# Optimization experiments

Measured on AMD Instinct MI355X. Metric: run time of the kernel, lower is better.

The kernel has to match this reference:

```python
import jax, jax.numpy as jnp
import numpy as np
from jax import lax

GAMMA = 0.1  # fixed RBF bandwidth from LearnableRBFInfluence


def setup_inputs() -> dict:
    key = jax.random.key(0)
    k1, k2, k3, k4 = jax.random.split(key, 4)
    B, H, W = 2, 256, 256
    NUM_FILTERS, KS, NUM_BASIS = 48, 7, 31
    u_log = jax.random.normal(k1, (B, 1, H, W), jnp.float32)
    f_log = jax.random.normal(k2, (B, 1, H, W), jnp.float32)
    filters = jax.random.normal(k3, (NUM_FILTERS, 1, KS, KS), jnp.float32) * 0.05
    rbf_weights = jax.random.normal(k4, (NUM_FILTERS, NUM_BASIS), jnp.float32) * 0.05
    lambda_param = jnp.float32(0.1)
    return {"u_log": u_log, "f_log": f_log, "filters": filters,
            "rbf_weights": rbf_weights, "lambda_param": lambda_param}


def reference(u_log, f_log, filters, rbf_weights, lambda_param):
    # Batched form of the per-filter loop:
    #   conv[i] = conv2d(u, k_i)  ->  one grouped conv with 48 output channels
    num_basis = rbf_weights.shape[1]
    mu = jnp.linspace(-1.0, 1.0, num_basis).astype(u_log.dtype)  # [K]

    dn = lax.conv_dimension_numbers(u_log.shape, filters.shape, ('NCHW', 'OIHW', 'NCHW'))
    conv = lax.conv_general_dilated(u_log, filters, (1, 1), 'SAME',
                                    dimension_numbers=dn)  # [B,48,H,W]

    # RBF influence, per filter channel c: phi = sum_k w[c,k] * exp(-(conv-mu_k)^2/(2 g^2))
    diff = conv[..., None] - mu                              # [B,48,H,W,K]
    rbf = jnp.exp(-(diff * diff) / (2.0 * GAMMA * GAMMA))
    phi = jnp.einsum('bchwk,ck->bchw', rbf, rbf_weights)     # [B,48,H,W]

    # Per-filter conv2d(phi_i, flip(k_i)) summed over i == single conv
    # with OIHW weight [1,48,7,7] built from spatially-flipped filters.
    kT = jnp.flip(filters, axis=(2, 3)).transpose(1, 0, 2, 3)  # [1,48,7,7]
    dn2 = lax.conv_dimension_numbers(phi.shape, kT.shape, ('NCHW', 'OIHW', 'NCHW'))
    diffusion = lax.conv_general_dilated(phi, kT, (1, 1), 'SAME',
                                         dimension_numbers=dn2)  # [B,1,H,W]

    reaction = lambda_param * (u_log - f_log)
    return u_log - diffusion - reaction
```

## Files before the change

kernel.cpp:

```cpp
#include <hip/hip_runtime.h>

#define HH 256
#define WW 256
#define NPIX (2 * HH * WW)
#define NC 48
#define NB 31
#define TP 192

#define OTY 32
#define OTX 64
#define PTY 38
#define PTX 70
#define PSTR2 76
#define UTY 44
#define UTX 76
#define USTR2 84
#define N1ITEM 684

#define OT 32
#define PT 38
#define PSTR 44
#define UT 44
#define USTR 52


__global__ __launch_bounds__(256)
void tnrd_table(const float* __restrict__ wr, float2* __restrict__ tab)
{
    const int ch = blockIdx.x;
    const float* rc = wr + ch * NB;
    for (int j = threadIdx.x; j < TP; j += 256) {
        float v0 = 0.f, v1 = 0.f;
        float x0 = fmaf((float)j, 1.0f / 64.0f, -1.5f);
        float x1 = x0 + 1.0f / 64.0f;
        #pragma unroll
        for (int k = 0; k < NB; ++k) {
            float mu = -1.f + (float)k * (1.f / 15.f);
            float d0 = x0 - mu, d1 = x1 - mu;
            float w = rc[k];
            v0 = fmaf(w, __expf(-50.f * d0 * d0), v0);
            v1 = fmaf(w, __expf(-50.f * d1 * d1), v1);
        }
        tab[ch * TP + j] = make_float2(v0, v1 - v0);
    }
}

#define F1STEP(WI, s0, s1, s2, s3)                                      \
    { float fa = wa[WI], fb = wb[WI];                                   \
      a0 = fmaf(s0, fa, a0); a1 = fmaf(s1, fa, a1);                     \
      a2 = fmaf(s2, fa, a2); a3 = fmaf(s3, fa, a3);                     \
      b0 = fmaf(s0, fb, b0); b1 = fmaf(s1, fb, b1);                     \
      b2 = fmaf(s2, fb, b2); b3 = fmaf(s3, fb, b3); }

#define F1ROW(WA, WB, q0, q1, q2)                                       \
    { const float* wa = (WA); const float* wb = (WB);                   \
      F1STEP(0, q0.x, q0.y, q0.z, q0.w)                                 \
      F1STEP(1, q0.y, q0.z, q0.w, q1.x)                                 \
      F1STEP(2, q0.z, q0.w, q1.x, q1.y)                                 \
      F1STEP(3, q0.w, q1.x, q1.y, q1.z)                                 \
      F1STEP(4, q1.x, q1.y, q1.z, q1.w)                                 \
      F1STEP(5, q1.y, q1.z, q1.w, q2.x)                                 \
      F1STEP(6, q1.z, q1.w, q2.x, q2.y) }

#define LERP1(res, aval, T)                                             \
    { float t_ = fminf(fmaxf(fmaf(aval, 64.f, 96.f), 0.f), 191.999f);   \
      float fj_ = floorf(t_);                                           \
      float2 e_ = (T)[(int)fj_];               \
      res = fmaf(t_ - fj_, e_.y, e_.x); }

#define C2STEPG(WI, s0, s1, s2, s3, t0, t1, t2, t3)                     \
    { float fa = wra[WI], fb = wrb[WI];                                 \
      q0 = fmaf(s0, fa, q0); q1 = fmaf(s1, fa, q1);                     \
      q2 = fmaf(s2, fa, q2); q3 = fmaf(s3, fa, q3);                     \
      q0 = fmaf(t0, fb, q0); q1 = fmaf(t1, fb, q1);                     \
      q2 = fmaf(t2, fb, q2); q3 = fmaf(t3, fb, q3); }

#define C2SWEEP()                                                       \
    C2STEPG(6, A0.x, A0.y, A0.z, A0.w, B0.x, B0.y, B0.z, B0.w)          \
    C2STEPG(5, A0.y, A0.z, A0.w, A1.x, B0.y, B0.z, B0.w, B1.x)          \
    C2STEPG(4, A0.z, A0.w, A1.x, A1.y, B0.z, B0.w, B1.x, B1.y)          \
    C2STEPG(3, A0.w, A1.x, A1.y, A1.z, B0.w, B1.x, B1.y, B1.z)          \
    C2STEPG(2, A1.x, A1.y, A1.z, A1.w, B1.x, B1.y, B1.z, B1.w)          \
    C2STEPG(1, A1.y, A1.z, A1.w, A2.x, B1.y, B1.z, B1.w, B2.x)          \
    C2STEPG(0, A1.z, A1.w, A2.x, A2.y, B1.z, B1.w, B2.x, B2.y)

__global__ __launch_bounds__(256, 4)
void tnrd_main_2x(const float* __restrict__ u,
                  const float* __restrict__ wf,
                  const float2* __restrict__ tab,
                  float* __restrict__ part)
{
    __shared__ __align__(16) float u_s[UTY * USTR2];
    __shared__ __align__(16) float phi_s[2][PTY * PSTR2];

    const int tid = threadIdx.x;
    const int bx = blockIdx.x, by = blockIdx.y;
    const int b = blockIdx.z / 24, g = blockIdx.z % 24;
    const int c0 = g * 2;

    const int uy0 = by * OTY - 6, ux0 = bx * OTX - 6;
    const float* ub = u + b * (HH * WW);
    for (int i = tid; i < UTY * USTR2; i += 256) {
        int r = i / USTR2, c = i - r * USTR2;
        int gy = uy0 + r, gx = ux0 + c;
        float v = 0.f;
        if (c < UTX && (unsigned)gy < HH && (unsigned)gx < WW)
            v = ub[gy * WW + gx];
        u_s[i] = v;
    }
    __syncthreads();

    const int py0 = by * OTY - 3, px0 = bx * OTX - 3;

    {
        const float* wA = wf + c0 * 49;
        const float* wB = wA + 49;
        const float2* tA = tab + c0 * TP;
        const float2* tB = tA + TP;
        for (int p = 0; p < 3; ++p) {
            const int gi = tid + p * 256;
            if (gi < N1ITEM) {
                const int pr = gi / 18, pc = (gi % 18) * 4;
                float a0 = 0.f, a1 = 0.f, a2 = 0.f, a3 = 0.f;
                float b0 = 0.f, b1 = 0.f, b2 = 0.f, b3 = 0.f;
                const float* bptr = &u_s[pr * USTR2 + pc];

                float4 c0v = *(const float4*)(bptr);
                float4 c1v = *(const float4*)(bptr + 4);
                float2 c2v = *(const float2*)(bptr + 8);
                #pragma unroll 1
                for (int dy = 0; dy < 6; ++dy) {
                    const float* nr = bptr + (dy + 1) * USTR2;
                    float4 n0 = *(const float4*)(nr);
                    float4 n1 = *(const float4*)(nr + 4);
                    float2 n2 = *(const float2*)(nr + 8);
                    F1ROW(wA + dy * 7, wB + dy * 7, c0v, c1v, c2v)
                    c0v = n0; c1v = n1; c2v = n2;
                }
                F1ROW(wA + 42, wB + 42, c0v, c1v, c2v)

                const int gy = py0 + pr;
                const bool rowok = (unsigned)gy < HH;
                const bool ok0 = rowok && (unsigned)(px0 + pc + 0) < WW;
                const bool ok1 = rowok && (unsigned)(px0 + pc + 1) < WW;
                const bool ok2 = rowok && (unsigned)(px0 + pc + 2) < WW;
                const bool ok3 = rowok && (unsigned)(px0 + pc + 3) < WW;
                float pA0, pA1, pA2, pA3, pB0, pB1, pB2, pB3;
                LERP1(pA0, a0, tA) LERP1(pB0, b0, tB)
                LERP1(pA1, a1, tA) LERP1(pB1, b1, tB)
                LERP1(pA2, a2, tA) LERP1(pB2, b2, tB)
                LERP1(pA3, a3, tA) LERP1(pB3, b3, tB)
                pA0 = ok0 ? pA0 : 0.f;  pB0 = ok0 ? pB0 : 0.f;
                pA1 = ok1 ? pA1 : 0.f;  pB1 = ok1 ? pB1 : 0.f;
                pA2 = ok2 ? pA2 : 0.f;  pB2 = ok2 ? pB2 : 0.f;
                pA3 = ok3 ? pA3 : 0.f;  pB3 = ok3 ? pB3 : 0.f;
                *(float4*)(&phi_s[0][pr * PSTR2 + pc]) =
                    make_float4(pA0, pA1, pA2, pA3);
                *(float4*)(&phi_s[1][pr * PSTR2 + pc]) =
                    make_float4(pB0, pB1, pB2, pB3);
            }
        }
    }
    __syncthreads();

    {
        const int tr = tid >> 4;
        const int ox = (tid & 15) * 4;
        const float* wA = wf + c0 * 49;
        const float* wB = wA + 49;
        float o00 = 0.f, o01 = 0.f, o02 = 0.f, o03 = 0.f;
        float o10 = 0.f, o11 = 0.f, o12 = 0.f, o13 = 0.f;

        #pragma unroll
        for (int dyt = 0; dyt < 8; ++dyt) {
            const float* rA = &phi_s[0][(2 * tr + dyt) * PSTR2 + ox];
            const float* rB = &phi_s[1][(2 * tr + dyt) * PSTR2 + ox];
            const float4 A0 = *(const float4*)(rA);
            const float4 A1 = *(const float4*)(rA + 4);
            const float2 A2 = *(const float2*)(rA + 8);
            const float4 B0 = *(const float4*)(rB);
            const float4 B1 = *(const float4*)(rB + 4);
            const float2 B2 = *(const float2*)(rB + 8);
            if (dyt < 7) {
                const float* wra = wA + (6 - dyt) * 7;
                const float* wrb = wB + (6 - dyt) * 7;
                float &q0 = o00, &q1 = o01, &q2 = o02, &q3 = o03;
                C2SWEEP()
            }
            if (dyt > 0) {
                const float* wra = wA + (7 - dyt) * 7;
                const float* wrb = wB + (7 - dyt) * 7;
                float &q0 = o10, &q1 = o11, &q2 = o12, &q3 = o13;
                C2SWEEP()
            }
        }

        const int gy0 = by * OTY + 2 * tr, gx = bx * OTX + ox;
        float* dst = part + (size_t)g * NPIX + b * (HH * WW) + gy0 * WW + gx;
        *reinterpret_cast<float4*>(dst)      = make_float4(o00, o01, o02, o03);
        *reinterpret_cast<float4*>(dst + WW) = make_float4(o10, o11, o12, o13);
    }
}

#define C2STEP(WI, s0, s1, s2, s3, t0, t1, t2, t3)                      \
    { float fa = wra[WI], fb = wrb[WI];                                 \
      o0 = fmaf(s0, fa, o0); o1 = fmaf(s1, fa, o1);                     \
      o2 = fmaf(s2, fa, o2); o3 = fmaf(s3, fa, o3);                     \
      o0 = fmaf(t0, fb, o0); o1 = fmaf(t1, fb, o1);                     \
      o2 = fmaf(t2, fb, o2); o3 = fmaf(t3, fb, o3); }

template<int CPG>
__global__ __launch_bounds__(256, 6)
void tnrd_main(const float* __restrict__ u,
               const float* __restrict__ wf,
               const float2* __restrict__ tab,
               float* __restrict__ part)
{
    constexpr int NGRP = NC / CPG;
    constexpr int NPASS = CPG / 2;
    __shared__ __align__(16) float u_s[UT * USTR];
    __shared__ __align__(16) float phi_s[2][PT * PSTR];

    const int tid = threadIdx.x;
    const int bx = blockIdx.x, by = blockIdx.y;
    const int b = blockIdx.z / NGRP, g = blockIdx.z % NGRP;
    const int c0g = g * CPG;

    const int uy0 = by * OT - 6, ux0 = bx * OT - 6;
    const float* ub = u + b * (HH * WW);
    for (int i = tid; i < UT * USTR; i += 256) {
        int r = i / USTR, c = i - r * USTR;
        int gy = uy0 + r, gx = ux0 + c;
        float v = 0.f;
        if (c < UT && (unsigned)gy < HH && (unsigned)gx < WW)
            v = ub[gy * WW + gx];
        u_s[i] = v;
    }
    __syncthreads();

    const int oy = tid >> 3;
    const int ox0 = (tid & 7) * 4;
    float o0 = 0.f, o1 = 0.f, o2 = 0.f, o3 = 0.f;
    const int py0 = by * OT - 3, px0 = bx * OT - 3;

    auto conv1_pass = [&](int cp, float* __restrict__ bufA,
                          float* __restrict__ bufB) {
        const float* wA = wf + (c0g + 2 * cp) * 49;
        const float* wB = wA + 49;
        const float2* tA = tab + (c0g + 2 * cp) * TP;
        const float2* tB = tA + TP;
        for (int p = 0; p < 2; ++p) {
            const int gi = tid + p * 256;
            if (gi < PT * 10) {
                const int pr = gi % PT, pc = (gi / PT) * 4;
                float a0 = 0.f, a1 = 0.f, a2 = 0.f, a3 = 0.f;
                float b0 = 0.f, b1 = 0.f, b2 = 0.f, b3 = 0.f;
                const float* bptr = &u_s[pr * USTR + pc];
                float4 c0 = *(const float4*)(bptr);
                float4 c1 = *(const float4*)(bptr + 4);
                float2 c2 = *(const float2*)(bptr + 8);
                #pragma unroll 1
                for (int dy = 0; dy < 6; ++dy) {
                    const float* nr = bptr + (dy + 1) * USTR;
                    float4 n0 = *(const float4*)(nr);
                    float4 n1 = *(const float4*)(nr + 4);
                    float2 n2 = *(const float2*)(nr + 8);
                    F1ROW(wA + dy * 7, wB + dy * 7, c0, c1, c2)
                    c0 = n0; c1 = n1; c2 = n2;
                }
                F1ROW(wA + 42, wB + 42, c0, c1, c2)
                const int gy = py0 + pr;
                const bool rowok = (unsigned)gy < HH;
                const bool ok0 = rowok && (unsigned)(px0 + pc + 0) < WW;
                const bool ok1 = rowok && (unsigned)(px0 + pc + 1) < WW;
                const bool ok2 = rowok && (unsigned)(px0 + pc + 2) < WW;
                const bool ok3 = rowok && (unsigned)(px0 + pc + 3) < WW;
                float pA0, pA1, pA2, pA3, pB0, pB1, pB2, pB3;
                LERP1(pA0, a0, tA) LERP1(pB0, b0, tB)
                LERP1(pA1, a1, tA) LERP1(pB1, b1, tB)
                LERP1(pA2, a2, tA) LERP1(pB2, b2, tB)
                LERP1(pA3, a3, tA) LERP1(pB3, b3, tB)
                pA0 = ok0 ? pA0 : 0.f;  pB0 = ok0 ? pB0 : 0.f;
                pA1 = ok1 ? pA1 : 0.f;  pB1 = ok1 ? pB1 : 0.f;
                pA2 = ok2 ? pA2 : 0.f;  pB2 = ok2 ? pB2 : 0.f;
                pA3 = ok3 ? pA3 : 0.f;  pB3 = ok3 ? pB3 : 0.f;
                *(float4*)(bufA + pr * PSTR + pc) =
                    make_float4(pA0, pA1, pA2, pA3);
                *(float4*)(bufB + pr * PSTR + pc) =
                    make_float4(pB0, pB1, pB2, pB3);
            }
        }
    };

    #pragma unroll 1
    for (int pass = 0; pass < NPASS; ++pass) {
        conv1_pass(pass, phi_s[0], phi_s[1]);
        __syncthreads();
        const float* wA = wf + (c0g + 2 * pass) * 49;
        const float* wB = wA + 49;
        const float* pA = phi_s[0];
        const float* pB = phi_s[1];
        for (int dy = 0; dy < 7; ++dy) {
            const float* rA = pA + (oy + dy) * PSTR + ox0;
            const float* rB = pB + (oy + dy) * PSTR + ox0;
            const float4 A0 = *(const float4*)(rA);
            const float4 A1 = *(const float4*)(rA + 4);
            const float2 A2 = *(const float2*)(rA + 8);
            const float4 B0 = *(const float4*)(rB);
            const float4 B1 = *(const float4*)(rB + 4);
            const float2 B2 = *(const float2*)(rB + 8);
            const float* wra = wA + (6 - dy) * 7;
            const float* wrb = wB + (6 - dy) * 7;
            C2STEP(6, A0.x, A0.y, A0.z, A0.w, B0.x, B0.y, B0.z, B0.w)
            C2STEP(5, A0.y, A0.z, A0.w, A1.x, B0.y, B0.z, B0.w, B1.x)
            C2STEP(4, A0.z, A0.w, A1.x, A1.y, B0.z, B0.w, B1.x, B1.y)
            C2STEP(3, A0.w, A1.x, A1.y, A1.z, B0.w, B1.x, B1.y, B1.z)
            C2STEP(2, A1.x, A1.y, A1.z, A1.w, B1.x, B1.y, B1.z, B1.w)
            C2STEP(1, A1.y, A1.z, A1.w, A2.x, B1.y, B1.z, B1.w, B2.x)
            C2STEP(0, A1.z, A1.w, A2.x, A2.y, B1.z, B1.w, B2.x, B2.y)
        }
        if (pass < NPASS - 1) __syncthreads();
    }

    const int gy = by * OT + oy, gx = bx * OT + ox0;
    float4 v4 = make_float4(o0, o1, o2, o3);
    *reinterpret_cast<float4*>(part + (size_t)g * NPIX + b * (HH * WW)
                               + gy * WW + gx) = v4;
}

template<int NGRP>
__global__ __launch_bounds__(256)
void combine_kernel(const float* __restrict__ u,
                    const float* __restrict__ f,
                    const float* __restrict__ lam,
                    const float* __restrict__ part,
                    float* __restrict__ out)
{
    int i = blockIdx.x * 256 + threadIdx.x;
    float d = 0.f;
    #pragma unroll
    for (int g = 0; g < NGRP; ++g) d += part[g * NPIX + i];
    float lv = lam[0];
    float uv = u[i];
    float fv = f[i];
    out[i] = uv - d - lv * (uv - fv);
}

extern "C" void kernel_launch(void* const* d_in, const int* in_sizes, int n_in,
                              void* d_out, int out_size, void* d_ws, size_t ws_size,
                              hipStream_t stream) {
    const float* u    = (const float*)d_in[0];
    const float* f    = (const float*)d_in[1];
    const float* filt = (const float*)d_in[2];
    const float* rbfw = (const float*)d_in[3];
    const float* lam  = (const float*)d_in[4];
    float* out = (float*)d_out;
    float* part = (float*)d_ws;
    float2* tabg = (float2*)d_out;

    tnrd_table<<<NC, 256, 0, stream>>>(rbfw, tabg);
    if (ws_size >= (size_t)24 * NPIX * sizeof(float)) {
        tnrd_main_2x<<<dim3(WW / OTX, HH / OTY, 48), 256, 0, stream>>>(
            u, filt, tabg, part);
        combine_kernel<24><<<512, 256, 0, stream>>>(u, f, lam, part, out);
    } else if (ws_size >= (size_t)12 * NPIX * sizeof(float)) {
        tnrd_main<4><<<dim3(8, 8, 24), 256, 0, stream>>>(u, filt, tabg, part);
        combine_kernel<12><<<512, 256, 0, stream>>>(u, f, lam, part, out);
    } else {
        tnrd_main<8><<<dim3(8, 8, 12), 256, 0, stream>>>(u, filt, tabg, part);
        combine_kernel<6><<<512, 256, 0, stream>>>(u, f, lam, part, out);
    }
}
```

Before: 101.9 us.

## Pre-pad input in global memory and read conv1 directly from it

A fused kernel now builds the RBF lookup table and writes a zero-padded copy of u into workspace. The main kernel drops its shared-memory staging of u and the barrier after it, and reads the first convolution's inputs from the padded global buffer with no bounds checks. Freeing that shared memory lets occupancy rise from 4 to 6 blocks per SM. The cost is an extra global write and read of the padded image, plus first-conv loads that now rely on L1/L2 caching instead of LDS.

```diff
diff --git a/kernel.cpp b/kernel.cpp
--- a/kernel.cpp
+++ b/kernel.cpp
@@ -10,12 +10,11 @@
 #define OTY 32
 #define OTX 64
 #define PTY 38
-#define PTX 70
 #define PSTR2 76
-#define UTY 44
-#define UTX 76
-#define USTR2 84
 #define N1ITEM 684
+
+#define PADW 272
+#define PADN (2 * PADW * PADW)
 
 #define OT 32
 #define PT 38
@@ -23,6 +22,42 @@
 #define UT 44
 #define USTR 52
 
+
+__global__ __launch_bounds__(256)
+void tnrd_table_pad(const float* __restrict__ wr,
+                    const float* __restrict__ u,
+                    float2* __restrict__ tab,
+                    float* __restrict__ upad)
+{
+    const int bid = blockIdx.x;
+    {
+        const int i = bid * 256 + threadIdx.x;
+        const int img = i / (PADW * PADW);
+        const int rem = i - img * (PADW * PADW);
+        const int py = rem / PADW, px = rem - py * PADW;
+        const int gy = py - 6, gx = px - 6;
+        float v = 0.f;
+        if ((unsigned)gy < HH && (unsigned)gx < WW)
+            v = u[img * (HH * WW) + gy * WW + gx];
+        upad[i] = v;
+    }
+    if (bid < NC && threadIdx.x < TP) {
+        const int j = threadIdx.x;
+        const float* rc = wr + bid * NB;
+        float v0 = 0.f, v1 = 0.f;
+        float x0 = fmaf((float)j, 1.0f / 64.0f, -1.5f);
+        float x1 = x0 + 1.0f / 64.0f;
+        #pragma unroll
+        for (int k = 0; k < NB; ++k) {
+            float mu = -1.f + (float)k * (1.f / 15.f);
+            float d0 = x0 - mu, d1 = x1 - mu;
+            float w = rc[k];
+            v0 = fmaf(w, __expf(-50.f * d0 * d0), v0);
+            v1 = fmaf(w, __expf(-50.f * d1 * d1), v1);
+        }
+        tab[bid * TP + j] = make_float2(v0, v1 - v0);
+    }
+}
 
 __global__ __launch_bounds__(256)
 void tnrd_table(const float* __restrict__ wr, float2* __restrict__ tab)
@@ -52,7 +87,7 @@
       b0 = fmaf(s0, fb, b0); b1 = fmaf(s1, fb, b1);                     \
       b2 = fmaf(s2, fb, b2); b3 = fmaf(s3, fb, b3); }
 
-#define F1ROW(WA, WB, q0, q1, q2)                                       \
+#define F1ROW(WA, WB, q0, q1, q2)                                      \
     { const float* wa = (WA); const float* wb = (WB);                   \
       F1STEP(0, q0.x, q0.y, q0.z, q0.w)                                 \
       F1STEP(1, q0.y, q0.z, q0.w, q1.x)                                 \
@@ -84,31 +119,18 @@
     C2STEPG(1, A1.y, A1.z, A1.w, A2.x, B1.y, B1.z, B1.w, B2.x)          \
     C2STEPG(0, A1.z, A1.w, A2.x, A2.y, B1.z, B1.w, B2.x, B2.y)
 
-__global__ __launch_bounds__(256, 4)
-void tnrd_main_2x(const float* __restrict__ u,
-                  const float* __restrict__ wf,
-                  const float2* __restrict__ tab,
-                  float* __restrict__ part)
+__global__ __launch_bounds__(256, 6)
+void tnrd_main_2xg(const float* __restrict__ upad,
+                   const float* __restrict__ wf,
+                   const float2* __restrict__ tab,
+                   float* __restrict__ part)
 {
-    __shared__ __align__(16) float u_s[UTY * USTR2];
     __shared__ __align__(16) float phi_s[2][PTY * PSTR2];
 
     const int tid = threadIdx.x;
     const int bx = blockIdx.x, by = blockIdx.y;
     const int b = blockIdx.z / 24, g = blockIdx.z % 24;
     const int c0 = g * 2;
-
-    const int uy0 = by * OTY - 6, ux0 = bx * OTX - 6;
-    const float* ub = u + b * (HH * WW);
-    for (int i = tid; i < UTY * USTR2; i += 256) {
-        int r = i / USTR2, c = i - r * USTR2;
-        int gy = uy0 + r, gx = ux0 + c;
-        float v = 0.f;
-        if (c < UTX && (unsigned)gy < HH && (unsigned)gx < WW)
-            v = ub[gy * WW + gx];
-        u_s[i] = v;
-    }
-    __syncthreads();
 
     const int py0 = by * OTY - 3, px0 = bx * OTX - 3;
 
@@ -117,20 +139,22 @@
         const float* wB = wA + 49;
         const float2* tA = tab + c0 * TP;
         const float2* tB = tA + TP;
+        const float* ubase = upad + b * (PADW * PADW);
         for (int p = 0; p < 3; ++p) {
             const int gi = tid + p * 256;
             if (gi < N1ITEM) {
                 const int pr = gi / 18, pc = (gi % 18) * 4;
                 float a0 = 0.f, a1 = 0.f, a2 = 0.f, a3 = 0.f;
                 float b0 = 0.f, b1 = 0.f, b2 = 0.f, b3 = 0.f;
-                const float* bptr = &u_s[pr * USTR2 + pc];
+                const float* bptr = ubase + (py0 + pr + 3) * PADW
+                                          + (bx * OTX + pc);
 
                 float4 c0v = *(const float4*)(bptr);
                 float4 c1v = *(const float4*)(bptr + 4);
                 float2 c2v = *(const float2*)(bptr + 8);
                 #pragma unroll 1
                 for (int dy = 0; dy < 6; ++dy) {
-                    const float* nr = bptr + (dy + 1) * USTR2;
+                    const float* nr = bptr + (dy + 1) * PADW;
                     float4 n0 = *(const float4*)(nr);
                     float4 n1 = *(const float4*)(nr + 4);
                     float2 n2 = *(const float2*)(nr + 8);
@@ -358,15 +382,19 @@
     float* part = (float*)d_ws;
     float2* tabg = (float2*)d_out;
 
-    tnrd_table<<<NC, 256, 0, stream>>>(rbfw, tabg);
-    if (ws_size >= (size_t)24 * NPIX * sizeof(float)) {
-        tnrd_main_2x<<<dim3(WW / OTX, HH / OTY, 48), 256, 0, stream>>>(
-            u, filt, tabg, part);
+    const size_t need = ((size_t)24 * NPIX + PADN) * sizeof(float);
+    if (ws_size >= need) {
+        float* upad = part + (size_t)24 * NPIX;
+        tnrd_table_pad<<<PADN / 256, 256, 0, stream>>>(rbfw, u, tabg, upad);
+        tnrd_main_2xg<<<dim3(WW / OTX, HH / OTY, 48), 256, 0, stream>>>(
+            upad, filt, tabg, part);
         combine_kernel<24><<<512, 256, 0, stream>>>(u, f, lam, part, out);
     } else if (ws_size >= (size_t)12 * NPIX * sizeof(float)) {
+        tnrd_table<<<NC, 256, 0, stream>>>(rbfw, tabg);
         tnrd_main<4><<<dim3(8, 8, 24), 256, 0, stream>>>(u, filt, tabg, part);
         combine_kernel<12><<<512, 256, 0, stream>>>(u, f, lam, part, out);
     } else {
+        tnrd_table<<<NC, 256, 0, stream>>>(rbfw, tabg);
         tnrd_main<8><<<dim3(8, 8, 12), 256, 0, stream>>>(u, filt, tabg, part);
         combine_kernel<6><<<512, 256, 0, stream>>>(u, f, lam, part, out);
     }
```

New measurement: 97.83 us. 1.04x faster.
